# Performance work log

Hardware: AMD Instinct MI355X
Metric: run time of the kernel (lower is better)

## Reference

```python
import jax, jax.numpy as jnp
import numpy as np

E, TOPK, H, F, CAP, TP = 8, 2, 1024, 4096, 2048, 1
N = 8192  # tokens * topk (token copies)


def setup_inputs() -> dict:
    key = jax.random.key(0)
    ks = jax.random.split(key, 6)
    inputs_shard = jax.random.normal(ks[0], (N, H), jnp.float32)
    gate_weight = jax.random.uniform(ks[1], (N,), jnp.float32)
    choosed_experts = jax.random.randint(ks[2], (N,), 0, E, dtype=jnp.int32)
    new_index = jax.random.permutation(ks[3], N).astype(jnp.int32)
    w1 = jax.random.normal(ks[4], (E, F, H), jnp.float32) * 0.02
    w2 = jax.random.normal(ks[5], (E, H, F), jnp.float32) * 0.02
    return {"inputs_shard": inputs_shard, "gate_weight": gate_weight,
            "choosed_experts": choosed_experts, "new_index": new_index,
            "w1": w1, "w2": w2}


def _grouped_expert_mlp(x, experts, w1, w2):
    # capacity-based grouped GEMM: sort token copies by expert, pack into
    # (E, CAP, H), run batched fc1->gelu->fc2, unpack back to token order.
    n = x.shape[0]
    order = jnp.argsort(experts)                      # [N]
    se = experts[order]
    offsets = jnp.searchsorted(se, jnp.arange(E))     # start of each expert block
    rank = jnp.arange(n) - offsets[se]                # within-expert position
    valid = rank < CAP                                # CAP=2*N/E, ~never drops
    slot = jnp.where(valid, se * CAP + rank, E * CAP) # out-of-range -> dropped
    buf = jnp.zeros((E * CAP, x.shape[1]), x.dtype).at[slot].set(x[order], mode="drop")
    xe = buf.reshape(E, CAP, -1)                      # [E, CAP, H]
    h = jax.nn.gelu(jnp.einsum("ech,efh->ecf", xe, w1), approximate=False)
    ye = jnp.einsum("ecf,ehf->ech", h, w2).reshape(E * CAP, -1)
    y_sorted = jnp.where(valid[:, None], ye[jnp.clip(slot, 0, E * CAP - 1)], 0.0)
    return jnp.zeros_like(x).at[order].set(y_sorted)  # back to token-copy order


def reference(inputs_shard, gate_weight, choosed_experts, new_index, w1, w2):
    # expert compute, scaled by router probabilities (combine-side scaling)
    result = _grouped_expert_mlp(inputs_shard, choosed_experts, w1, w2)
    result = result * gate_weight[:, None]
    # scatter combine: output1[new_index] = result; full_output += output1
    full_output = jnp.zeros((N, H), result.dtype).at[new_index].set(result)
    # topk reduce: view(N//topk, topk, H).sum(1)
    topk_reduce = full_output.reshape(N // TOPK, TOPK, H).sum(1)
    # reduce_scatter over TP group; TP=1 => identity
    return topk_reduce
```

## Files before the change

### kernel.cpp

```cpp
#include <hip/hip_runtime.h>
#include <stdint.h>

#define N_TOK 8192
#define HDIM  1024
#define FDIM  4096
#define NEXP  8
#define MAXTILES 72
#define MAXT256  40

typedef __attribute__((ext_vector_type(8))) __bf16 bf16x8;
typedef __attribute__((ext_vector_type(8))) unsigned short ushort8v;
typedef __attribute__((ext_vector_type(4))) unsigned short ushort4v;
typedef __attribute__((ext_vector_type(4))) float floatx4;

__device__ __forceinline__ unsigned short f2bf(float f) {
  union { float f; uint32_t u; } v; v.f = f;
  uint32_t u = v.u;
  return (unsigned short)((u + 0x7FFFu + ((u >> 16) & 1u)) >> 16);
}

__device__ __forceinline__ void load_lds16(const void* g, void* l) {
  __builtin_amdgcn_global_load_lds(
      (const __attribute__((address_space(1))) void*)(uintptr_t)g,
      (__attribute__((address_space(3))) void*)(uint32_t)(uintptr_t)l,
      16, 0, 0);
}


__global__ void k_count(const int* __restrict__ experts, int* __restrict__ meta) {
  int i = blockIdx.x * 256 + threadIdx.x;
  atomicAdd(&meta[experts[i]], 1);
}

__global__ void k_plan(int* __restrict__ meta) {
  if (threadIdx.x == 0) {
    int off = 0, nt = 0, nt2 = 0;
    for (int e = 0; e < NEXP; ++e) {
      int c = meta[e];
      meta[8 + e] = off;
      meta[16 + e] = off;
      int t = (c + 127) >> 7;
      for (int k = 0; k < t; ++k) meta[32 + nt++] = (e << 16) | k;
      int t2 = (c + 255) >> 8;
      for (int k = 0; k < t2; ++k) meta[104 + nt2++] = (e << 16) | k;
      off += c;
    }
    meta[24] = nt;
    meta[25] = nt2;
  }
}

__global__ void k_scatter(const int* __restrict__ experts, int* __restrict__ meta,
                          int* __restrict__ order) {
  int i = blockIdx.x * 256 + threadIdx.x;
  int e = experts[i];
  int pos = atomicAdd(&meta[16 + e], 1);
  order[pos] = i;
}

__global__ void k_pack(const float* __restrict__ x, const int* __restrict__ order,
                       unsigned short* __restrict__ xs) {
  int s = blockIdx.x;
  int i = order[s];
  int t = threadIdx.x;
  float4 v = *(const float4*)(x + (size_t)i * HDIM + t * 4);
  ushort4v u;
  u[0] = f2bf(v.x); u[1] = f2bf(v.y); u[2] = f2bf(v.z); u[3] = f2bf(v.w);
  *(ushort4v*)(xs + (size_t)s * HDIM + t * 4) = u;
}

__global__ void k_cvt(const float* __restrict__ src, unsigned short* __restrict__ dst) {
  size_t i = ((size_t)blockIdx.x * 256 + threadIdx.x) * 4;
  float4 v = *(const float4*)(src + i);
  ushort4v u;
  u[0] = f2bf(v.x); u[1] = f2bf(v.y); u[2] = f2bf(v.z); u[3] = f2bf(v.w);
  *(ushort4v*)(dst + i) = u;
}


#define VM_WAIT(n) asm volatile("s_waitcnt vmcnt(" #n ")" ::: "memory")

__global__ __launch_bounds__(512, 1) void gemm1_big(
    const unsigned short* __restrict__ xs, const unsigned short* __restrict__ wb,
    unsigned short* __restrict__ h1, const int* __restrict__ meta) {
  __shared__ unsigned short As[2][256 * 64];
  __shared__ unsigned short Bs[2][256 * 64];

  int bx = blockIdx.z;
  if (bx >= meta[25]) return;
  int entry = meta[104 + bx];
  int e = entry >> 16, mt = entry & 0xffff;
  int row0 = meta[8 + e] + mt * 256;
  int rend = meta[8 + e] + meta[e];
  int fBase = blockIdx.x * 256;

  int tid = threadIdx.x;
  int w = tid >> 6, l = tid & 63;
  int r = l & 15, q = l >> 4;

  int srow = w * 8 + (l >> 3);
  int scol = ((l & 7) ^ (l >> 3)) << 3;
  const unsigned short* aP[4];
  const unsigned short* bP[4];
#pragma unroll
  for (int n = 0; n < 4; ++n) {
    int ar = min(row0 + n * 64 + srow, N_TOK - 1);
    aP[n] = xs + (size_t)ar * HDIM + scol;
    int br = fBase + n * 64 + srow;
    bP[n] = wb + ((size_t)e * FDIM + br) * HDIM + scol;
  }

  floatx4 acc[8][4];
#pragma unroll
  for (int i = 0; i < 8; ++i)
#pragma unroll
    for (int j = 0; j < 4; ++j) acc[i][j] = (floatx4){0.f, 0.f, 0.f, 0.f};

  int mb = (w >> 2) * 128;
  int nb = (w & 3) * 64;

  {
#pragma unroll
    for (int n = 0; n < 4; ++n) load_lds16(aP[n], &As[0][n * 4096 + w * 512]);
#pragma unroll
    for (int n = 0; n < 4; ++n) load_lds16(bP[n], &Bs[0][n * 4096 + w * 512]);
  }

  const int NT = HDIM / 64;
  for (int kt = 0; kt < NT; ++kt) {
    int cur = kt & 1;
    if (kt + 1 < NT) {
      int ko = (kt + 1) * 64;
      int nxt = cur ^ 1;
#pragma unroll
      for (int n = 0; n < 4; ++n) load_lds16(aP[n] + ko, &As[nxt][n * 4096 + w * 512]);
#pragma unroll
      for (int n = 0; n < 4; ++n) load_lds16(bP[n] + ko, &Bs[nxt][n * 4096 + w * 512]);
      VM_WAIT(8);
    } else {
      VM_WAIT(0);
    }
    __builtin_amdgcn_s_barrier();
    __builtin_amdgcn_sched_barrier(0);

#pragma unroll
    for (int kk = 0; kk < 2; ++kk) {
      bf16x8 av[8], bv[4];
#pragma unroll
      for (int i = 0; i < 8; ++i) {
        int row = mb + i * 16 + r;
        int col = (kk * 32 + q * 8) ^ ((r & 7) << 3);
        av[i] = __builtin_bit_cast(bf16x8, *(const ushort8v*)&As[cur][row * 64 + col]);
      }
#pragma unroll
      for (int j = 0; j < 4; ++j) {
        int row = nb + j * 16 + r;
        int col = (kk * 32 + q * 8) ^ ((r & 7) << 3);
        bv[j] = __builtin_bit_cast(bf16x8, *(const ushort8v*)&Bs[cur][row * 64 + col]);
      }
      __builtin_amdgcn_s_setprio(1);
#pragma unroll
      for (int i = 0; i < 8; ++i)
#pragma unroll
        for (int j = 0; j < 4; ++j)
          acc[i][j] = __builtin_amdgcn_mfma_f32_16x16x32_bf16(av[i], bv[j], acc[i][j], 0, 0, 0);
      __builtin_amdgcn_s_setprio(0);
    }
    __builtin_amdgcn_s_barrier();
  }

#pragma unroll
  for (int i = 0; i < 8; ++i) {
    int mrow = row0 + mb + i * 16 + q * 4;
#pragma unroll
    for (int reg = 0; reg < 4; ++reg) {
      int s = mrow + reg;
      if (s < rend) {
        unsigned short* dst = h1 + (size_t)s * FDIM + fBase + nb + r;
#pragma unroll
        for (int j = 0; j < 4; ++j) {
          float v = acc[i][j][reg];
          float g = 0.5f * v * (1.0f + erff(v * 0.70710678118654752f));
          dst[j * 16] = f2bf(g);
        }
      }
    }
  }
}

__global__ __launch_bounds__(512, 1) void gemm2_big(
    const unsigned short* __restrict__ h1, const unsigned short* __restrict__ wb,
    const float* __restrict__ gate, const int* __restrict__ new_index,
    float* __restrict__ out, const int* __restrict__ meta) {
  __shared__ unsigned short As[2][256 * 64];
  __shared__ unsigned short Bs[2][128 * 64];

  int bx = blockIdx.z;
  if (bx >= meta[25]) return;
  int entry = meta[104 + bx];
  int e = entry >> 16, mt = entry & 0xffff;
  int row0 = meta[8 + e] + mt * 256;
  int rend = meta[8 + e] + meta[e];
  int nBase = blockIdx.x * 128;
  int kStart = blockIdx.y * (FDIM / 2);
  const int* order = meta + 256;

  int tid = threadIdx.x;
  int w = tid >> 6, l = tid & 63;
  int r = l & 15, q = l >> 4;

  int srow = w * 8 + (l >> 3);
  int scol = ((l & 7) ^ (l >> 3)) << 3;
  const unsigned short* aP[4];
  const unsigned short* bP[2];
#pragma unroll
  for (int n = 0; n < 4; ++n) {
    int ar = min(row0 + n * 64 + srow, N_TOK - 1);
    aP[n] = h1 + (size_t)ar * FDIM + kStart + scol;
  }
#pragma unroll
  for (int n = 0; n < 2; ++n) {
    int br = nBase + n * 64 + srow;
    bP[n] = wb + ((size_t)e * HDIM + br) * FDIM + kStart + scol;
  }

  floatx4 acc[4][4];
#pragma unroll
  for (int i = 0; i < 4; ++i)
#pragma unroll
    for (int j = 0; j < 4; ++j) acc[i][j] = (floatx4){0.f, 0.f, 0.f, 0.f};

  int mb = (w >> 1) * 64;
  int nb = (w & 1) * 64;

  {
#pragma unroll
    for (int n = 0; n < 4; ++n) load_lds16(aP[n], &As[0][n * 4096 + w * 512]);
#pragma unroll
    for (int n = 0; n < 2; ++n) load_lds16(bP[n], &Bs[0][n * 4096 + w * 512]);
  }

  const int NT = (FDIM / 2) / 64;
  for (int kt = 0; kt < NT; ++kt) {
    int cur = kt & 1;
    if (kt + 1 < NT) {
      int ko = (kt + 1) * 64;
      int nxt = cur ^ 1;
#pragma unroll
      for (int n = 0; n < 4; ++n) load_lds16(aP[n] + ko, &As[nxt][n * 4096 + w * 512]);
#pragma unroll
      for (int n = 0; n < 2; ++n) load_lds16(bP[n] + ko, &Bs[nxt][n * 4096 + w * 512]);
      VM_WAIT(6);
    } else {
      VM_WAIT(0);
    }
    __builtin_amdgcn_s_barrier();
    __builtin_amdgcn_sched_barrier(0);

#pragma unroll
    for (int kk = 0; kk < 2; ++kk) {
      bf16x8 av[4], bv[4];
#pragma unroll
      for (int i = 0; i < 4; ++i) {
        int row = mb + i * 16 + r;
        int col = (kk * 32 + q * 8) ^ ((r & 7) << 3);
        av[i] = __builtin_bit_cast(bf16x8, *(const ushort8v*)&As[cur][row * 64 + col]);
      }
#pragma unroll
      for (int j = 0; j < 4; ++j) {
        int row = nb + j * 16 + r;
        int col = (kk * 32 + q * 8) ^ ((r & 7) << 3);
        bv[j] = __builtin_bit_cast(bf16x8, *(const ushort8v*)&Bs[cur][row * 64 + col]);
      }
      __builtin_amdgcn_s_setprio(1);
#pragma unroll
      for (int i = 0; i < 4; ++i)
#pragma unroll
        for (int j = 0; j < 4; ++j)
          acc[i][j] = __builtin_amdgcn_mfma_f32_16x16x32_bf16(av[i], bv[j], acc[i][j], 0, 0, 0);
      __builtin_amdgcn_s_setprio(0);
    }
    __builtin_amdgcn_s_barrier();
  }

#pragma unroll
  for (int i = 0; i < 4; ++i) {
    int mrow = row0 + mb + i * 16 + q * 4;
#pragma unroll
    for (int reg = 0; reg < 4; ++reg) {
      int s = mrow + reg;
      if (s < rend) {
        int itok = order[s];
        float gw = gate[itok];
        int jdx = new_index[itok];
        float* dst = out + (size_t)(jdx >> 1) * HDIM + nBase + nb + r;
#pragma unroll
        for (int j = 0; j < 4; ++j) atomicAdd(dst + j * 16, acc[i][j][reg] * gw);
      }
    }
  }
}


template <bool PRE>
__global__ __launch_bounds__(256) void gemm1_t(
    const unsigned short* __restrict__ xs, const void* __restrict__ w1v,
    unsigned short* __restrict__ h1, const int* __restrict__ meta) {
  __shared__ unsigned short As[128 * 32];
  __shared__ unsigned short Bs[128 * 32];

  int bx = blockIdx.z;
  if (bx >= meta[24]) return;
  int entry = meta[32 + bx];
  int e = entry >> 16, mt = entry & 0xffff;
  int row0 = meta[8 + e] + mt * 128;
  int rend = meta[8 + e] + meta[e];
  int fBase = blockIdx.x * 128;

  int tid = threadIdx.x;
  int w = tid >> 6, lane = tid & 63;
  int r = lane & 15, q = lane >> 4;
  int wm = (w >> 1) * 64, wn = (w & 1) * 64;

  int ar0 = (w * 16) + (lane >> 2);
  int s0 = min(row0 + ar0, N_TOK - 1);
  int s1 = min(row0 + 64 + ar0, N_TOK - 1);
  const unsigned short* ag0 = xs + (size_t)s0 * HDIM + (lane & 3) * 8;
  const unsigned short* ag1 = xs + (size_t)s1 * HDIM + (lane & 3) * 8;
  unsigned short* al0 = &As[(w * 16) * 32];
  unsigned short* al1 = &As[(64 + w * 16) * 32];

  const float* wbase = nullptr; int brow = 0, bkk = 0;
  brow = tid >> 1; bkk = (tid & 1) * 16;
  wbase = (const float*)w1v + ((size_t)e * FDIM + fBase + brow) * HDIM + bkk;

  floatx4 acc[4][4];
#pragma unroll
  for (int i = 0; i < 4; ++i)
#pragma unroll
    for (int j = 0; j < 4; ++j) acc[i][j] = (floatx4){0.f, 0.f, 0.f, 0.f};

  for (int k0 = 0; k0 < HDIM; k0 += 32) {
    __syncthreads();
    load_lds16(ag0 + k0, al0);
    load_lds16(ag1 + k0, al1);
    {
      const float* gb = wbase + k0;
      float4 f0 = *(const float4*)(gb);
      float4 f1 = *(const float4*)(gb + 4);
      float4 f2 = *(const float4*)(gb + 8);
      float4 f3 = *(const float4*)(gb + 12);
      ushort8v u0, u1;
      u0[0] = f2bf(f0.x); u0[1] = f2bf(f0.y); u0[2] = f2bf(f0.z); u0[3] = f2bf(f0.w);
      u0[4] = f2bf(f1.x); u0[5] = f2bf(f1.y); u0[6] = f2bf(f1.z); u0[7] = f2bf(f1.w);
      u1[0] = f2bf(f2.x); u1[1] = f2bf(f2.y); u1[2] = f2bf(f2.z); u1[3] = f2bf(f2.w);
      u1[4] = f2bf(f3.x); u1[5] = f2bf(f3.y); u1[6] = f2bf(f3.z); u1[7] = f2bf(f3.w);
      *(ushort8v*)&Bs[brow * 32 + bkk] = u0;
      *(ushort8v*)&Bs[brow * 32 + bkk + 8] = u1;
    }
    __syncthreads();

    bf16x8 av[4], bv[4];
#pragma unroll
    for (int i = 0; i < 4; ++i)
      av[i] = __builtin_bit_cast(bf16x8, *(const ushort8v*)&As[(wm + i * 16 + r) * 32 + q * 8]);
#pragma unroll
    for (int j = 0; j < 4; ++j)
      bv[j] = __builtin_bit_cast(bf16x8, *(const ushort8v*)&Bs[(wn + j * 16 + r) * 32 + q * 8]);
#pragma unroll
    for (int i = 0; i < 4; ++i)
#pragma unroll
      for (int j = 0; j < 4; ++j)
        acc[i][j] = __builtin_amdgcn_mfma_f32_16x16x32_bf16(av[i], bv[j], acc[i][j], 0, 0, 0);
  }

#pragma unroll
  for (int i = 0; i < 4; ++i) {
    int mrow = row0 + wm + i * 16 + q * 4;
#pragma unroll
    for (int reg = 0; reg < 4; ++reg) {
      int s = mrow + reg;
      if (s < rend) {
        unsigned short* dst = h1 + (size_t)s * FDIM + fBase + wn + r;
#pragma unroll
        for (int j = 0; j < 4; ++j) {
          float v = acc[i][j][reg];
          float g = 0.5f * v * (1.0f + erff(v * 0.70710678118654752f));
          dst[j * 16] = f2bf(g);
        }
      }
    }
  }
}

template <bool PRE>
__global__ __launch_bounds__(256) void gemm2_t(
    const unsigned short* __restrict__ h1, const void* __restrict__ w2v,
    const float* __restrict__ gate, const int* __restrict__ new_index,
    float* __restrict__ out, const int* __restrict__ meta) {
  __shared__ unsigned short As[128 * 32];
  __shared__ unsigned short Bs[128 * 32];

  int bx = blockIdx.z;
  if (bx >= meta[24]) return;
  int entry = meta[32 + bx];
  int e = entry >> 16, mt = entry & 0xffff;
  int row0 = meta[8 + e] + mt * 128;
  int rend = meta[8 + e] + meta[e];
  int nBase = blockIdx.x * 128;
  int kStart = blockIdx.y * (FDIM / 2);
  int kEnd = kStart + (FDIM / 2);
  const int* order = meta + 256;

  int tid = threadIdx.x;
  int w = tid >> 6, lane = tid & 63;
  int r = lane & 15, q = lane >> 4;
  int wm = (w >> 1) * 64, wn = (w & 1) * 64;

  int ar0 = (w * 16) + (lane >> 2);
  int s0 = min(row0 + ar0, N_TOK - 1);
  int s1 = min(row0 + 64 + ar0, N_TOK - 1);
  const unsigned short* ag0 = h1 + (size_t)s0 * FDIM + (lane & 3) * 8;
  const unsigned short* ag1 = h1 + (size_t)s1 * FDIM + (lane & 3) * 8;
  unsigned short* al0 = &As[(w * 16) * 32];
  unsigned short* al1 = &As[(64 + w * 16) * 32];

  const float* wbase = nullptr; int brow = 0, bkk = 0;
  brow = tid >> 1; bkk = (tid & 1) * 16;
  wbase = (const float*)w2v + ((size_t)e * HDIM + nBase + brow) * FDIM + bkk;

  floatx4 acc[4][4];
#pragma unroll
  for (int i = 0; i < 4; ++i)
#pragma unroll
    for (int j = 0; j < 4; ++j) acc[i][j] = (floatx4){0.f, 0.f, 0.f, 0.f};

  for (int k0 = kStart; k0 < kEnd; k0 += 32) {
    __syncthreads();
    load_lds16(ag0 + k0, al0);
    load_lds16(ag1 + k0, al1);
    {
      const float* gb = wbase + k0;
      float4 f0 = *(const float4*)(gb);
      float4 f1 = *(const float4*)(gb + 4);
      float4 f2 = *(const float4*)(gb + 8);
      float4 f3 = *(const float4*)(gb + 12);
      ushort8v u0, u1;
      u0[0] = f2bf(f0.x); u0[1] = f2bf(f0.y); u0[2] = f2bf(f0.z); u0[3] = f2bf(f0.w);
      u0[4] = f2bf(f1.x); u0[5] = f2bf(f1.y); u0[6] = f2bf(f1.z); u0[7] = f2bf(f1.w);
      u1[0] = f2bf(f2.x); u1[1] = f2bf(f2.y); u1[2] = f2bf(f2.z); u1[3] = f2bf(f2.w);
      u1[4] = f2bf(f3.x); u1[5] = f2bf(f3.y); u1[6] = f2bf(f3.z); u1[7] = f2bf(f3.w);
      *(ushort8v*)&Bs[brow * 32 + bkk] = u0;
      *(ushort8v*)&Bs[brow * 32 + bkk + 8] = u1;
    }
    __syncthreads();

    bf16x8 av[4], bv[4];
#pragma unroll
    for (int i = 0; i < 4; ++i)
      av[i] = __builtin_bit_cast(bf16x8, *(const ushort8v*)&As[(wm + i * 16 + r) * 32 + q * 8]);
#pragma unroll
    for (int j = 0; j < 4; ++j)
      bv[j] = __builtin_bit_cast(bf16x8, *(const ushort8v*)&Bs[(wn + j * 16 + r) * 32 + q * 8]);
#pragma unroll
    for (int i = 0; i < 4; ++i)
#pragma unroll
      for (int j = 0; j < 4; ++j)
        acc[i][j] = __builtin_amdgcn_mfma_f32_16x16x32_bf16(av[i], bv[j], acc[i][j], 0, 0, 0);
  }

#pragma unroll
  for (int i = 0; i < 4; ++i) {
    int mrow = row0 + wm + i * 16 + q * 4;
#pragma unroll
    for (int reg = 0; reg < 4; ++reg) {
      int s = mrow + reg;
      if (s < rend) {
        int itok = order[s];
        float gw = gate[itok];
        int jdx = new_index[itok];
        float* dst = out + (size_t)(jdx >> 1) * HDIM + nBase + wn + r;
#pragma unroll
        for (int j = 0; j < 4; ++j) atomicAdd(dst + j * 16, acc[i][j][reg] * gw);
      }
    }
  }
}

extern "C" void kernel_launch(void* const* d_in, const int* in_sizes, int n_in,
                              void* d_out, int out_size, void* d_ws, size_t ws_size,
                              hipStream_t stream) {
  const float* x        = (const float*)d_in[0];
  const float* gate     = (const float*)d_in[1];
  const int* experts    = (const int*)d_in[2];
  const int* new_index  = (const int*)d_in[3];
  const float* w1       = (const float*)d_in[4];
  const float* w2       = (const float*)d_in[5];
  float* out            = (float*)d_out;

  int* meta = (int*)d_ws;
  int* order = meta + 256;
  const size_t XS_OFF = 65536;
  const size_t XS_SZ  = (size_t)N_TOK * HDIM * 2;
  const size_t H1_SZ  = (size_t)N_TOK * FDIM * 2;
  const size_t W_SZ   = (size_t)NEXP * FDIM * HDIM * 2;
  unsigned short* xs  = (unsigned short*)((char*)d_ws + XS_OFF);
  unsigned short* h1  = (unsigned short*)((char*)d_ws + XS_OFF + XS_SZ);
  unsigned short* w1b = (unsigned short*)((char*)d_ws + XS_OFF + XS_SZ + H1_SZ);
  unsigned short* w2b = (unsigned short*)((char*)d_ws + XS_OFF + XS_SZ + H1_SZ + W_SZ);
  size_t need_small = XS_OFF + XS_SZ + H1_SZ;
  size_t need_big   = need_small + 2 * W_SZ;
  if (ws_size < need_small) return;
  bool big = ws_size >= need_big;

  hipMemsetAsync(d_ws, 0, 4096, stream);
  hipMemsetAsync(d_out, 0, (size_t)out_size * sizeof(float), stream);
  k_count<<<N_TOK / 256, 256, 0, stream>>>(experts, meta);
  k_plan<<<1, 64, 0, stream>>>(meta);
  k_scatter<<<N_TOK / 256, 256, 0, stream>>>(experts, meta, order);
  k_pack<<<N_TOK, 256, 0, stream>>>(x, order, xs);

  if (big) {
    int nblk = (int)((size_t)NEXP * FDIM * HDIM / 4 / 256);
    k_cvt<<<nblk, 256, 0, stream>>>(w1, w1b);
    k_cvt<<<nblk, 256, 0, stream>>>(w2, w2b);
    gemm1_big<<<dim3(FDIM / 256, 1, MAXT256), 512, 0, stream>>>(xs, w1b, h1, meta);
    gemm2_big<<<dim3(HDIM / 128, 2, MAXT256), 512, 0, stream>>>(h1, w2b, gate, new_index, out, meta);
  } else {
    gemm1_t<false><<<dim3(FDIM / 128, 1, MAXTILES), 256, 0, stream>>>(xs, w1, h1, meta);
    gemm2_t<false><<<dim3(HDIM / 128, 2, MAXTILES), 256, 0, stream>>>(h1, w2, gate, new_index, out, meta);
  }
}
```

Baseline: 698.9 us.

## Unify expert GEMMs into one templated kernel with triple-buffered LDS pipeline

Replaces the two big-path GEMM kernels with one templated kernel using a 256x128 tile and a three-stage LDS ring buffer. The prefetch is issued two tiles ahead, after the barrier, which removes the trailing barrier per k-step. GEMM1 moves from 256x256 tiles to 256x128, which doubles its grid and cuts registers and LDS per block, at the cost of re-reading the A tile more often. The GELU and atomic-combine epilogues are picked at compile time. LDS use rises to 144KB per block, which may limit occupancy.

```diff
diff --git a/kernel.cpp b/kernel.cpp
--- a/kernel.cpp
+++ b/kernel.cpp
@@ -80,120 +80,14 @@
 
 #define VM_WAIT(n) asm volatile("s_waitcnt vmcnt(" #n ")" ::: "memory")
 
-__global__ __launch_bounds__(512, 1) void gemm1_big(
-    const unsigned short* __restrict__ xs, const unsigned short* __restrict__ wb,
-    unsigned short* __restrict__ h1, const int* __restrict__ meta) {
-  __shared__ unsigned short As[2][256 * 64];
-  __shared__ unsigned short Bs[2][256 * 64];
-
-  int bx = blockIdx.z;
-  if (bx >= meta[25]) return;
-  int entry = meta[104 + bx];
-  int e = entry >> 16, mt = entry & 0xffff;
-  int row0 = meta[8 + e] + mt * 256;
-  int rend = meta[8 + e] + meta[e];
-  int fBase = blockIdx.x * 256;
-
-  int tid = threadIdx.x;
-  int w = tid >> 6, l = tid & 63;
-  int r = l & 15, q = l >> 4;
-
-  int srow = w * 8 + (l >> 3);
-  int scol = ((l & 7) ^ (l >> 3)) << 3;
-  const unsigned short* aP[4];
-  const unsigned short* bP[4];
-#pragma unroll
-  for (int n = 0; n < 4; ++n) {
-    int ar = min(row0 + n * 64 + srow, N_TOK - 1);
-    aP[n] = xs + (size_t)ar * HDIM + scol;
-    int br = fBase + n * 64 + srow;
-    bP[n] = wb + ((size_t)e * FDIM + br) * HDIM + scol;
-  }
-
-  floatx4 acc[8][4];
-#pragma unroll
-  for (int i = 0; i < 8; ++i)
-#pragma unroll
-    for (int j = 0; j < 4; ++j) acc[i][j] = (floatx4){0.f, 0.f, 0.f, 0.f};
-
-  int mb = (w >> 2) * 128;
-  int nb = (w & 3) * 64;
-
-  {
-#pragma unroll
-    for (int n = 0; n < 4; ++n) load_lds16(aP[n], &As[0][n * 4096 + w * 512]);
-#pragma unroll
-    for (int n = 0; n < 4; ++n) load_lds16(bP[n], &Bs[0][n * 4096 + w * 512]);
-  }
-
-  const int NT = HDIM / 64;
-  for (int kt = 0; kt < NT; ++kt) {
-    int cur = kt & 1;
-    if (kt + 1 < NT) {
-      int ko = (kt + 1) * 64;
-      int nxt = cur ^ 1;
-#pragma unroll
-      for (int n = 0; n < 4; ++n) load_lds16(aP[n] + ko, &As[nxt][n * 4096 + w * 512]);
-#pragma unroll
-      for (int n = 0; n < 4; ++n) load_lds16(bP[n] + ko, &Bs[nxt][n * 4096 + w * 512]);
-      VM_WAIT(8);
-    } else {
-      VM_WAIT(0);
-    }
-    __builtin_amdgcn_s_barrier();
-    __builtin_amdgcn_sched_barrier(0);
-
-#pragma unroll
-    for (int kk = 0; kk < 2; ++kk) {
-      bf16x8 av[8], bv[4];
-#pragma unroll
-      for (int i = 0; i < 8; ++i) {
-        int row = mb + i * 16 + r;
-        int col = (kk * 32 + q * 8) ^ ((r & 7) << 3);
-        av[i] = __builtin_bit_cast(bf16x8, *(const ushort8v*)&As[cur][row * 64 + col]);
-      }
-#pragma unroll
-      for (int j = 0; j < 4; ++j) {
-        int row = nb + j * 16 + r;
-        int col = (kk * 32 + q * 8) ^ ((r & 7) << 3);
-        bv[j] = __builtin_bit_cast(bf16x8, *(const ushort8v*)&Bs[cur][row * 64 + col]);
-      }
-      __builtin_amdgcn_s_setprio(1);
-#pragma unroll
-      for (int i = 0; i < 8; ++i)
-#pragma unroll
-        for (int j = 0; j < 4; ++j)
-          acc[i][j] = __builtin_amdgcn_mfma_f32_16x16x32_bf16(av[i], bv[j], acc[i][j], 0, 0, 0);
-      __builtin_amdgcn_s_setprio(0);
-    }
-    __builtin_amdgcn_s_barrier();
-  }
-
-#pragma unroll
-  for (int i = 0; i < 8; ++i) {
-    int mrow = row0 + mb + i * 16 + q * 4;
-#pragma unroll
-    for (int reg = 0; reg < 4; ++reg) {
-      int s = mrow + reg;
-      if (s < rend) {
-        unsigned short* dst = h1 + (size_t)s * FDIM + fBase + nb + r;
-#pragma unroll
-        for (int j = 0; j < 4; ++j) {
-          float v = acc[i][j][reg];
-          float g = 0.5f * v * (1.0f + erff(v * 0.70710678118654752f));
-          dst[j * 16] = f2bf(g);
-        }
-      }
-    }
-  }
-}
-
-__global__ __launch_bounds__(512, 1) void gemm2_big(
-    const unsigned short* __restrict__ h1, const unsigned short* __restrict__ wb,
-    const float* __restrict__ gate, const int* __restrict__ new_index,
-    float* __restrict__ out, const int* __restrict__ meta) {
-  __shared__ unsigned short As[2][256 * 64];
-  __shared__ unsigned short Bs[2][128 * 64];
+template <int K_TOTAL, int NT, int EPI>
+__global__ __launch_bounds__(512, 1) void gemm_big(
+    const unsigned short* __restrict__ A, const unsigned short* __restrict__ B,
+    unsigned short* __restrict__ h1out, const float* __restrict__ gate,
+    const int* __restrict__ new_index, float* __restrict__ out,
+    const int* __restrict__ meta) {
+  __shared__ unsigned short As[3][256 * 64];
+  __shared__ unsigned short Bs[3][128 * 64];
 
   int bx = blockIdx.z;
   if (bx >= meta[25]) return;
@@ -202,8 +96,7 @@
   int row0 = meta[8 + e] + mt * 256;
   int rend = meta[8 + e] + meta[e];
   int nBase = blockIdx.x * 128;
-  int kStart = blockIdx.y * (FDIM / 2);
-  const int* order = meta + 256;
+  int kStart = blockIdx.y * (NT * 64);
 
   int tid = threadIdx.x;
   int w = tid >> 6, l = tid & 63;
@@ -216,12 +109,12 @@
 #pragma unroll
   for (int n = 0; n < 4; ++n) {
     int ar = min(row0 + n * 64 + srow, N_TOK - 1);
-    aP[n] = h1 + (size_t)ar * FDIM + kStart + scol;
+    aP[n] = A + (size_t)ar * K_TOTAL + kStart + scol;
   }
 #pragma unroll
   for (int n = 0; n < 2; ++n) {
     int br = nBase + n * 64 + srow;
-    bP[n] = wb + ((size_t)e * HDIM + br) * FDIM + kStart + scol;
+    bP[n] = B + (size_t)e * 4194304 + (size_t)br * K_TOTAL + kStart + scol;
   }
 
   floatx4 acc[4][4];
@@ -233,29 +126,29 @@
   int mb = (w >> 1) * 64;
   int nb = (w & 1) * 64;
 
-  {
-#pragma unroll
-    for (int n = 0; n < 4; ++n) load_lds16(aP[n], &As[0][n * 4096 + w * 512]);
-#pragma unroll
-    for (int n = 0; n < 2; ++n) load_lds16(bP[n], &Bs[0][n * 4096 + w * 512]);
-  }
-
-  const int NT = (FDIM / 2) / 64;
+#pragma unroll
+  for (int n = 0; n < 4; ++n) load_lds16(aP[n], &As[0][n * 4096 + w * 512]);
+#pragma unroll
+  for (int n = 0; n < 2; ++n) load_lds16(bP[n], &Bs[0][n * 4096 + w * 512]);
+#pragma unroll
+  for (int n = 0; n < 4; ++n) load_lds16(aP[n] + 64, &As[1][n * 4096 + w * 512]);
+#pragma unroll
+  for (int n = 0; n < 2; ++n) load_lds16(bP[n] + 64, &Bs[1][n * 4096 + w * 512]);
+
+  int cur = 0;
   for (int kt = 0; kt < NT; ++kt) {
-    int cur = kt & 1;
-    if (kt + 1 < NT) {
-      int ko = (kt + 1) * 64;
-      int nxt = cur ^ 1;
-#pragma unroll
-      for (int n = 0; n < 4; ++n) load_lds16(aP[n] + ko, &As[nxt][n * 4096 + w * 512]);
-#pragma unroll
-      for (int n = 0; n < 2; ++n) load_lds16(bP[n] + ko, &Bs[nxt][n * 4096 + w * 512]);
-      VM_WAIT(6);
-    } else {
-      VM_WAIT(0);
-    }
+    if (kt == NT - 1) { VM_WAIT(0); } else { VM_WAIT(6); }
     __builtin_amdgcn_s_barrier();
     __builtin_amdgcn_sched_barrier(0);
+
+    if (kt + 2 < NT) {
+      int stg = cur + 2; if (stg >= 3) stg -= 3;
+      int ko = (kt + 2) * 64;
+#pragma unroll
+      for (int n = 0; n < 4; ++n) load_lds16(aP[n] + ko, &As[stg][n * 4096 + w * 512]);
+#pragma unroll
+      for (int n = 0; n < 2; ++n) load_lds16(bP[n] + ko, &Bs[stg][n * 4096 + w * 512]);
+    }
 
 #pragma unroll
     for (int kk = 0; kk < 2; ++kk) {
@@ -280,22 +173,44 @@
           acc[i][j] = __builtin_amdgcn_mfma_f32_16x16x32_bf16(av[i], bv[j], acc[i][j], 0, 0, 0);
       __builtin_amdgcn_s_setprio(0);
     }
-    __builtin_amdgcn_s_barrier();
-  }
-
-#pragma unroll
-  for (int i = 0; i < 4; ++i) {
-    int mrow = row0 + mb + i * 16 + q * 4;
-#pragma unroll
-    for (int reg = 0; reg < 4; ++reg) {
-      int s = mrow + reg;
-      if (s < rend) {
-        int itok = order[s];
-        float gw = gate[itok];
-        int jdx = new_index[itok];
-        float* dst = out + (size_t)(jdx >> 1) * HDIM + nBase + nb + r;
-#pragma unroll
-        for (int j = 0; j < 4; ++j) atomicAdd(dst + j * 16, acc[i][j][reg] * gw);
+
+    ++cur; if (cur >= 3) cur = 0;
+  }
+
+  if constexpr (EPI == 0) {
+#pragma unroll
+    for (int i = 0; i < 4; ++i) {
+      int mrow = row0 + mb + i * 16 + q * 4;
+#pragma unroll
+      for (int reg = 0; reg < 4; ++reg) {
+        int s = mrow + reg;
+        if (s < rend) {
+          unsigned short* dst = h1out + (size_t)s * FDIM + nBase + nb + r;
+#pragma unroll
+          for (int j = 0; j < 4; ++j) {
+            float v = acc[i][j][reg];
+            float g = 0.5f * v * (1.0f + erff(v * 0.70710678118654752f));
+            dst[j * 16] = f2bf(g);
+          }
+        }
+      }
+    }
+  } else {
+    const int* order = meta + 256;
+#pragma unroll
+    for (int i = 0; i < 4; ++i) {
+      int mrow = row0 + mb + i * 16 + q * 4;
+#pragma unroll
+      for (int reg = 0; reg < 4; ++reg) {
+        int s = mrow + reg;
+        if (s < rend) {
+          int itok = order[s];
+          float gw = gate[itok];
+          int jdx = new_index[itok];
+          float* dst = out + (size_t)(jdx >> 1) * HDIM + nBase + nb + r;
+#pragma unroll
+          for (int j = 0; j < 4; ++j) atomicAdd(dst + j * 16, acc[i][j][reg] * gw);
+        }
       }
     }
   }
@@ -524,8 +439,10 @@
     int nblk = (int)((size_t)NEXP * FDIM * HDIM / 4 / 256);
     k_cvt<<<nblk, 256, 0, stream>>>(w1, w1b);
     k_cvt<<<nblk, 256, 0, stream>>>(w2, w2b);
-    gemm1_big<<<dim3(FDIM / 256, 1, MAXT256), 512, 0, stream>>>(xs, w1b, h1, meta);
-    gemm2_big<<<dim3(HDIM / 128, 2, MAXT256), 512, 0, stream>>>(h1, w2b, gate, new_index, out, meta);
+    gemm_big<HDIM, 16, 0><<<dim3(FDIM / 128, 1, MAXT256), 512, 0, stream>>>(
+        xs, w1b, h1, nullptr, nullptr, nullptr, meta);
+    gemm_big<FDIM, 32, 1><<<dim3(HDIM / 128, 2, MAXT256), 512, 0, stream>>>(
+        h1, w2b, nullptr, gate, new_index, out, meta);
   } else {
     gemm1_t<false><<<dim3(FDIM / 128, 1, MAXTILES), 256, 0, stream>>>(xs, w1, h1, meta);
     gemm2_t<false><<<dim3(HDIM / 128, 2, MAXTILES), 256, 0, stream>>>(h1, w2, gate, new_index, out, meta);
```

New measurement: 676.5 us. 1.03x faster.
